# Performance work log

Measured on AMD Instinct MI355X. Metric: run time of the kernel, lower is better.

The kernel has to match this reference:

```python
import jax, jax.numpy as jnp
import numpy as np

N_NODES = 100000
N_EDGES = 1600000
D = 128
N_GRAPHS = 128
N_LAYERS = 3


def setup_inputs() -> dict:
    key = jax.random.key(0)
    ks = jax.random.split(key, 3 + 4 * N_LAYERS)
    x = jax.random.normal(ks[0], (N_NODES, D), dtype=jnp.float32)
    edge_index = jax.random.randint(ks[1], (2, N_EDGES), 0, N_NODES, dtype=jnp.int64)
    batch = jnp.sort(jax.random.randint(ks[2], (N_NODES,), 0, N_GRAPHS, dtype=jnp.int64))
    inp = {"x": x, "edge_index": edge_index, "batch": batch}
    scale = 1.0 / np.sqrt(D)
    for l in range(N_LAYERS):
        inp[f"W1_{l}"] = jax.random.normal(ks[3 + 4 * l], (D, D), dtype=jnp.float32) * scale
        inp[f"b1_{l}"] = jnp.zeros((D,), dtype=jnp.float32)
        inp[f"W2_{l}"] = jax.random.normal(ks[4 + 4 * l], (D, D), dtype=jnp.float32) * scale
        inp[f"b2_{l}"] = jnp.zeros((D,), dtype=jnp.float32)
    return inp


def _gin_conv(x, edge_index, W1, b1, W2, b2):
    # GINConv with eps=0: out = MLP(x + sum_{j in N(i)} x_j)
    msgs = x[edge_index[0]]                                   # [E, D] gather
    agg = jax.ops.segment_sum(msgs, edge_index[1], num_segments=N_NODES)
    h = x + agg
    h = jax.nn.relu(h @ W1 + b1)
    return h @ W2 + b2


def reference(x, edge_index, batch,
              W1_0, b1_0, W2_0, b2_0,
              W1_1, b1_1, W2_1, b2_1,
              W1_2, b1_2, W2_2, b2_2):
    params = [(W1_0, b1_0, W2_0, b2_0), (W1_1, b1_1, W2_1, b2_1), (W1_2, b1_2, W2_2, b2_2)]
    h = x
    for l in range(N_LAYERS - 1):
        h = _gin_conv(h, edge_index, *params[l])
        h = jax.nn.relu(h)  # act; dropout with drop_ratio=0 is identity
    node_emb = _gin_conv(h, edge_index, *params[-1])  # JK='last'
    # global_mean_pool
    sums = jax.ops.segment_sum(node_emb, batch, num_segments=N_GRAPHS)
    counts = jax.ops.segment_sum(jnp.ones((N_NODES, 1), node_emb.dtype), batch, num_segments=N_GRAPHS)
    graph_emb = sums / jnp.maximum(counts, 1.0)
    return graph_emb
```

## Files before the change

### kernel.cpp

```cpp
#include <hip/hip_runtime.h>
#include <hip/hip_bf16.h>

#define N_NODES 100000
#define N_PAD   100032
#define N_EDGES 1600000
#define DIM 128
#define N_GRAPHS 128
#define NBKT 98
#define BSTRIDE 18432
#define TILES (N_PAD / 16)
#define GRID_MLP 1024
#define POOL_BLKS ((N_NODES + 127) / 128)
#define B1_BATCH 4096
#define B1_GRID ((N_EDGES + B1_BATCH - 1) / B1_BATCH)

typedef unsigned short u16;
typedef unsigned int u32;
typedef __attribute__((ext_vector_type(8))) short bf16x8;
typedef __attribute__((ext_vector_type(4))) float f32x4;

#define MFMA(A, B, C) __builtin_amdgcn_mfma_f32_16x16x32_bf16(A, B, C, 0, 0, 0)

__device__ __forceinline__ u16 f2bf(float x) {
    u32 u = __float_as_uint(x);
    u = (u + 0x7FFFu + ((u >> 16) & 1u)) >> 16;
    return (u16)u;
}
__device__ __forceinline__ float bf2f(u16 u) {
    return __uint_as_float(((u32)u) << 16);
}

__global__ __launch_bounds__(256) void bucket1_kernel(const int* __restrict__ src,
                                                      const int* __restrict__ dst,
                                                      u32* __restrict__ cursorB,
                                                      u32* __restrict__ pairs) {
    __shared__ int lh[NBKT];
    __shared__ u32 lbase[NBKT];
    int t = threadIdx.x;
    if (t < NBKT) lh[t] = 0;
    __syncthreads();
    int e0 = blockIdx.x * B1_BATCH;
    int d[16], s[16], rk[16];
#pragma unroll
    for (int k = 0; k < 16; ++k) {
        int e = e0 + t + k * 256;
        if (e < N_EDGES) {
            d[k] = dst[e];
            s[k] = src[e];
            rk[k] = atomicAdd(&lh[d[k] >> 10], 1);
        }
    }
    __syncthreads();
    if (t < NBKT) lbase[t] = atomicAdd(&cursorB[t], (u32)lh[t]) + (u32)(t * BSTRIDE);
    __syncthreads();
#pragma unroll
    for (int k = 0; k < 16; ++k) {
        int e = e0 + t + k * 256;
        if (e < N_EDGES) {
            u32 pos = lbase[d[k] >> 10] + (u32)rk[k];
            pairs[pos] = ((u32)(d[k] & 1023) << 22) | (u32)s[k];
        }
    }
}

__global__ __launch_bounds__(1024) void bucket2_kernel(const u32* __restrict__ cursorB,
                                                       const u32* __restrict__ pairs,
                                                       int* __restrict__ row_ptr,
                                                       int* __restrict__ csr) {
    __shared__ int lh[1024];
    __shared__ int rc[1024];
    __shared__ int bs[128];
    int b = blockIdx.x, t = threadIdx.x;

    if (t < 128) bs[t] = (t < NBKT) ? (int)cursorB[t] : 0;
    __syncthreads();
    for (int off = 1; off < 128; off <<= 1) {
        int v = (t < 128 && t >= off) ? bs[t - off] : 0;
        __syncthreads();
        if (t < 128) bs[t] += v;
        __syncthreads();
    }
    int cnt = (int)cursorB[b];
    int bbase = (b == 0) ? 0 : bs[b - 1];

    lh[t] = 0;
    __syncthreads();
    const u32* pb = pairs + (size_t)b * BSTRIDE;
    for (int i = t; i < cnt; i += 1024) atomicAdd(&lh[__builtin_nontemporal_load(pb + i) >> 22], 1);
    __syncthreads();

    int own = lh[t];
    for (int off = 1; off < 1024; off <<= 1) {
        int v = (t >= off) ? lh[t - off] : 0;
        __syncthreads();
        lh[t] += v;
        __syncthreads();
    }
    int excl = lh[t] - own;
    int node = b * 1024 + t;
    if (node < N_NODES) row_ptr[node] = bbase + excl;
    if (b == 0 && t == 0) row_ptr[N_NODES] = N_EDGES;
    rc[t] = bbase + excl;
    __syncthreads();

    for (int i = t; i < cnt; i += 1024) {
        u32 p = __builtin_nontemporal_load(pb + i);
        int pos = atomicAdd(&rc[p >> 22], 1);
        csr[pos] = (int)(p & 0x3FFFFFu);
    }
}

__global__ __launch_bounds__(256) void xprep_kernel(const float* __restrict__ x,
                                                    u16* __restrict__ hb) {
    int i = blockIdx.x * 256 + threadIdx.x;
    if (i < N_NODES * 32) {
        float4 v = ((const float4*)x)[i];
        ushort4 o;
        o.x = f2bf(v.x); o.y = f2bf(v.y); o.z = f2bf(v.z); o.w = f2bf(v.w);
        ((ushort4*)hb)[i] = o;
    }
}

__global__ __launch_bounds__(256) void agg_kernel(const u16* __restrict__ hb,
                                                  const int* __restrict__ rp,
                                                  const int* __restrict__ csr,
                                                  u16* __restrict__ Ah,
                                                  u16* __restrict__ Al) {
    int node = (blockIdx.x * 256 + threadIdx.x) >> 5;
    int l = threadIdx.x & 31;
    if (node >= N_NODES) return;
    const ushort4* h4 = (const ushort4*)hb;
    ushort4 sv = h4[(size_t)node * 32 + l];
    float a0 = bf2f(sv.x), a1 = bf2f(sv.y), a2 = bf2f(sv.z), a3 = bf2f(sv.w);
    int s = rp[node], e = rp[node + 1];
    int i = s;
    for (; i + 8 <= e; i += 8) {
        ushort4 v0 = h4[(size_t)csr[i + 0] * 32 + l];
        ushort4 v1 = h4[(size_t)csr[i + 1] * 32 + l];
        ushort4 v2 = h4[(size_t)csr[i + 2] * 32 + l];
        ushort4 v3 = h4[(size_t)csr[i + 3] * 32 + l];
        ushort4 v4 = h4[(size_t)csr[i + 4] * 32 + l];
        ushort4 v5 = h4[(size_t)csr[i + 5] * 32 + l];
        ushort4 v6 = h4[(size_t)csr[i + 6] * 32 + l];
        ushort4 v7 = h4[(size_t)csr[i + 7] * 32 + l];
        a0 += ((bf2f(v0.x) + bf2f(v1.x)) + (bf2f(v2.x) + bf2f(v3.x))) +
              ((bf2f(v4.x) + bf2f(v5.x)) + (bf2f(v6.x) + bf2f(v7.x)));
        a1 += ((bf2f(v0.y) + bf2f(v1.y)) + (bf2f(v2.y) + bf2f(v3.y))) +
              ((bf2f(v4.y) + bf2f(v5.y)) + (bf2f(v6.y) + bf2f(v7.y)));
        a2 += ((bf2f(v0.z) + bf2f(v1.z)) + (bf2f(v2.z) + bf2f(v3.z))) +
              ((bf2f(v4.z) + bf2f(v5.z)) + (bf2f(v6.z) + bf2f(v7.z)));
        a3 += ((bf2f(v0.w) + bf2f(v1.w)) + (bf2f(v2.w) + bf2f(v3.w))) +
              ((bf2f(v4.w) + bf2f(v5.w)) + (bf2f(v6.w) + bf2f(v7.w)));
    }
    for (; i < e; ++i) {
        ushort4 v = h4[(size_t)csr[i] * 32 + l];
        a0 += bf2f(v.x); a1 += bf2f(v.y); a2 += bf2f(v.z); a3 += bf2f(v.w);
    }
    ushort4 hv, lv;
    hv.x = f2bf(a0); lv.x = f2bf(a0 - bf2f(hv.x));
    hv.y = f2bf(a1); lv.y = f2bf(a1 - bf2f(hv.y));
    hv.z = f2bf(a2); lv.z = f2bf(a2 - bf2f(hv.z));
    hv.w = f2bf(a3); lv.w = f2bf(a3 - bf2f(hv.w));
    *(ushort4*)(Ah + (size_t)node * 128 + l * 4) = hv;
    *(ushort4*)(Al + (size_t)node * 128 + l * 4) = lv;
}

struct WPrepArgs {
    const float* w[6];
    u16* buf[6];
};
__global__ __launch_bounds__(256) void wprep_kernel(WPrepArgs p) {
    int m = blockIdx.y;
    int idx = blockIdx.x * 256 + threadIdx.x;
    int n = idx >> 7, k = idx & 127;
    float v = p.w[m][k * 128 + n];
    u16 hi = f2bf(v);
    p.buf[m][idx] = hi;
    p.buf[m][idx + 16384] = f2bf(v - bf2f(hi));
}

#define HS 136
__global__ __launch_bounds__(256, 2) void fused_mlp(const u16* __restrict__ Ah,
                                                    const u16* __restrict__ Al,
                                                    const u16* __restrict__ W1,
                                                    const float* __restrict__ b1,
                                                    const u16* __restrict__ W2,
                                                    const float* __restrict__ b2,
                                                    float* __restrict__ Cf,
                                                    u16* __restrict__ Cb, int mode) {
    __shared__ u16 Hh[32 * HS];
    __shared__ u16 Hl[32 * HS];
    int tid = threadIdx.x;
    int lane = tid & 63, wave = tid >> 6;
    int m16 = lane & 15, quad = lane >> 4;
    int colBase = wave * 32;

    bf16x8 W1H[2][4], W1L[2][4], W2H[2][4], W2L[2][4];
#pragma unroll
    for (int nt = 0; nt < 2; ++nt) {
        int n = colBase + nt * 16 + m16;
#pragma unroll
        for (int kb = 0; kb < 4; ++kb) {
            int off = n * 128 + kb * 32 + quad * 8;
            W1H[nt][kb] = *(const bf16x8*)(W1 + off);
            W1L[nt][kb] = *(const bf16x8*)(W1 + off + 16384);
            W2H[nt][kb] = *(const bf16x8*)(W2 + off);
            W2L[nt][kb] = *(const bf16x8*)(W2 + off + 16384);
        }
    }
    float b1v[2][4], b2v[2][4];
#pragma unroll
    for (int nt = 0; nt < 2; ++nt)
#pragma unroll
        for (int rg = 0; rg < 4; ++rg) {
            int col = colBase + nt * 16 + quad * 4 + rg;
            b1v[nt][rg] = b1[col];
            b2v[nt][rg] = b2[col];
        }

    f32x4 z = {0.f, 0.f, 0.f, 0.f};
    bf16x8 aH[2][4], aL[2][4];

    int t0 = blockIdx.x * 2;
    if (t0 < TILES) {
#pragma unroll
        for (int p = 0; p < 2; ++p) {
            const u16* ah = Ah + (size_t)((t0 + p) * 16 + m16) * 128 + quad * 8;
            const u16* al = Al + (size_t)((t0 + p) * 16 + m16) * 128 + quad * 8;
#pragma unroll
            for (int kb = 0; kb < 4; ++kb) {
                aH[p][kb] = *(const bf16x8*)(ah + kb * 32);
                aL[p][kb] = *(const bf16x8*)(al + kb * 32);
            }
        }
    }

    for (; t0 < TILES; t0 += 2 * GRID_MLP) {
        f32x4 acc[2][2];
        acc[0][0] = z; acc[0][1] = z; acc[1][0] = z; acc[1][1] = z;

#pragma unroll
        for (int kb = 0; kb < 4; ++kb) {
#pragma unroll
            for (int p = 0; p < 2; ++p) {
                acc[p][0] = MFMA(W1H[0][kb], aH[p][kb], acc[p][0]);
                acc[p][1] = MFMA(W1H[1][kb], aH[p][kb], acc[p][1]);
                acc[p][0] = MFMA(W1H[0][kb], aL[p][kb], acc[p][0]);
                acc[p][1] = MFMA(W1H[1][kb], aL[p][kb], acc[p][1]);
                acc[p][0] = MFMA(W1L[0][kb], aH[p][kb], acc[p][0]);
                acc[p][1] = MFMA(W1L[1][kb], aH[p][kb], acc[p][1]);
            }
        }

        __syncthreads();

#pragma unroll
        for (int p = 0; p < 2; ++p) {
#pragma unroll
            for (int nt = 0; nt < 2; ++nt) {
                ushort4 hv, lv;
#pragma unroll
                for (int rg = 0; rg < 4; ++rg) {
                    float v = fmaxf(acc[p][nt][rg] + b1v[nt][rg], 0.f);
                    u16 hi = f2bf(v);
                    ((u16*)&hv)[rg] = hi;
                    ((u16*)&lv)[rg] = f2bf(v - bf2f(hi));
                }
                int off = (p * 16 + m16) * HS + colBase + nt * 16 + quad * 4;
                *(ushort4*)&Hh[off] = hv;
                *(ushort4*)&Hl[off] = lv;
            }
        }
        __syncthreads();

        int nt0 = t0 + 2 * GRID_MLP;
        if (nt0 < TILES) {
#pragma unroll
            for (int p = 0; p < 2; ++p) {
                const u16* ah = Ah + (size_t)((nt0 + p) * 16 + m16) * 128 + quad * 8;
                const u16* al = Al + (size_t)((nt0 + p) * 16 + m16) * 128 + quad * 8;
#pragma unroll
                for (int kb = 0; kb < 4; ++kb) {
                    aH[p][kb] = *(const bf16x8*)(ah + kb * 32);
                    aL[p][kb] = *(const bf16x8*)(al + kb * 32);
                }
            }
        }

        f32x4 acc2[2][2];
        acc2[0][0] = z; acc2[0][1] = z; acc2[1][0] = z; acc2[1][1] = z;
#pragma unroll
        for (int kb = 0; kb < 4; ++kb) {
#pragma unroll
            for (int p = 0; p < 2; ++p) {
                int off = (p * 16 + m16) * HS + kb * 32 + quad * 8;
                bf16x8 hH = *(const bf16x8*)(&Hh[off]);
                bf16x8 hL = *(const bf16x8*)(&Hl[off]);
                acc2[p][0] = MFMA(W2H[0][kb], hH, acc2[p][0]);
                acc2[p][1] = MFMA(W2H[1][kb], hH, acc2[p][1]);
                acc2[p][0] = MFMA(W2H[0][kb], hL, acc2[p][0]);
                acc2[p][1] = MFMA(W2H[1][kb], hL, acc2[p][1]);
                acc2[p][0] = MFMA(W2L[0][kb], hH, acc2[p][0]);
                acc2[p][1] = MFMA(W2L[1][kb], hH, acc2[p][1]);
            }
        }

#pragma unroll
        for (int p = 0; p < 2; ++p) {
            size_t row = (size_t)(t0 + p) * 16 + m16;
#pragma unroll
            for (int nt = 0; nt < 2; ++nt) {
                int col = colBase + nt * 16 + quad * 4;
                if (mode) {
                    ushort4 o;
#pragma unroll
                    for (int rg = 0; rg < 4; ++rg)
                        ((u16*)&o)[rg] = f2bf(fmaxf(acc2[p][nt][rg] + b2v[nt][rg], 0.f));
                    *(ushort4*)(Cb + row * 128 + col) = o;
                } else {
                    float4 o;
                    o.x = acc2[p][nt][0] + b2v[nt][0];
                    o.y = acc2[p][nt][1] + b2v[nt][1];
                    o.z = acc2[p][nt][2] + b2v[nt][2];
                    o.w = acc2[p][nt][3] + b2v[nt][3];
                    *(float4*)(Cf + row * 128 + col) = o;
                }
            }
        }
    }
}

__global__ __launch_bounds__(256) void psum_kernel(const float* __restrict__ h,
                                                   const int* __restrict__ batch,
                                                   float* __restrict__ sums) {
    __shared__ int sBatch[128];
    int blk = blockIdx.x, t = threadIdx.x;
    int n0 = blk * 128;
    int nEnd = min(n0 + 128, N_NODES);
    if (t < 128 && n0 + t < N_NODES) sBatch[t] = batch[n0 + t];
    __syncthreads();

    int j = t & 127;
    int half = t >> 7;
    int s = n0 + half * 64;
    int e = min(s + 64, nEnd);

    float acc = 0.f;
    int cur = -1;
    for (int n = s; n < e; ++n) {
        int g = sBatch[n - n0];
        if (g != cur) {
            if (cur >= 0) atomicAdd(&sums[cur * 128 + j], acc);
            cur = g;
            acc = 0.f;
        }
        acc += h[(size_t)n * 128 + j];
    }
    if (cur >= 0) atomicAdd(&sums[cur * 128 + j], acc);
}

__global__ __launch_bounds__(128) void pdiv_kernel(const float* __restrict__ sums,
                                                   const int* __restrict__ batch,
                                                   float* __restrict__ out) {
    __shared__ int sB[2];
    int g = blockIdx.x;
    if (threadIdx.x < 2) {
        int target = g + threadIdx.x;
        int lo = 0, hi = N_NODES;
        while (lo < hi) {
            int m = (lo + hi) >> 1;
            if (batch[m] < target) lo = m + 1; else hi = m;
        }
        sB[threadIdx.x] = lo;
    }
    __syncthreads();
    float cnt = (float)(sB[1] - sB[0]);
    out[g * 128 + threadIdx.x] = sums[g * 128 + threadIdx.x] / fmaxf(cnt, 1.f);
}

extern "C" void kernel_launch(void* const* d_in, const int* in_sizes, int n_in,
                              void* d_out, int out_size, void* d_ws, size_t ws_size,
                              hipStream_t stream) {
    const float* x     = (const float*)d_in[0];
    const int*   ei    = (const int*)d_in[1];
    const int*   batch = (const int*)d_in[2];
    const int*   eSrc  = ei;
    const int*   eDst  = ei + N_EDGES;

    const float* W1[3] = {(const float*)d_in[3], (const float*)d_in[7],  (const float*)d_in[11]};
    const float* b1[3] = {(const float*)d_in[4], (const float*)d_in[8],  (const float*)d_in[12]};
    const float* W2[3] = {(const float*)d_in[5], (const float*)d_in[9],  (const float*)d_in[13]};
    const float* b2[3] = {(const float*)d_in[6], (const float*)d_in[10], (const float*)d_in[14]};

    float* P2 = (float*)d_ws;
    u16*   hb = (u16*)(P2 + (size_t)N_PAD * DIM);
    u16*   Ah = hb + (size_t)N_PAD * DIM;
    u16*   Al = Ah + (size_t)N_PAD * DIM;
    u16*   Wb = Al + (size_t)N_PAD * DIM;
    int*   row_ptr = (int*)(Wb + 6 * 32768);
    u32*   cursorB = (u32*)(row_ptr + N_NODES + 8);
    int*   csr     = (int*)(cursorB + 128);
    float* sums    = (float*)(csr + N_EDGES);
    u32*   pairs   = (u32*)P2;

    hipMemsetAsync(cursorB, 0, 128 * sizeof(u32), stream);
    bucket1_kernel<<<B1_GRID, 256, 0, stream>>>(eSrc, eDst, cursorB, pairs);
    bucket2_kernel<<<NBKT, 1024, 0, stream>>>(cursorB, pairs, row_ptr, csr);

    xprep_kernel<<<(N_NODES * 32 + 255) / 256, 256, 0, stream>>>(x, hb);
    WPrepArgs wp;
    for (int l = 0; l < 3; ++l) {
        wp.w[2 * l]       = W1[l];
        wp.w[2 * l + 1]   = W2[l];
        wp.buf[2 * l]     = Wb + (size_t)(2 * l) * 32768;
        wp.buf[2 * l + 1] = Wb + (size_t)(2 * l + 1) * 32768;
    }
    wprep_kernel<<<dim3(64, 6), 256, 0, stream>>>(wp);
    hipMemsetAsync(sums, 0, N_GRAPHS * DIM * sizeof(float), stream);

    const int aggGrid = (N_NODES * 32 + 255) / 256;

    for (int l = 0; l < 3; ++l) {
        agg_kernel<<<aggGrid, 256, 0, stream>>>(hb, row_ptr, csr, Ah, Al);
        fused_mlp<<<GRID_MLP, 256, 0, stream>>>(Ah, Al,
                                                Wb + (size_t)(2 * l) * 32768, b1[l],
                                                Wb + (size_t)(2 * l + 1) * 32768, b2[l],
                                                P2, hb, (l < 2) ? 1 : 0);
    }
    psum_kernel<<<POOL_BLKS, 256, 0, stream>>>(P2, batch, sums);
    pdiv_kernel<<<N_GRAPHS, 128, 0, stream>>>(sums, batch, (float*)d_out);
}
```

Measured before the change: 532.1 us.

## Drop low-half bf16 split of aggregated activations and process four tiles per block

The aggregation kernel now writes only the bf16 high part of the summed features, so the separate low-residual buffer and its stores and loads are removed. The first MLP GEMM goes from three MFMA passes to two (W-hi×A and W-lo×A). The fused MLP block also handles four 16-row tiles per iteration instead of two, with larger shared buffers. This cuts memory traffic and MFMA work, but at the cost of precision in the first layer's input, and raises register and LDS use, which may lower occupancy.

```diff
diff --git a/kernel.cpp b/kernel.cpp
--- a/kernel.cpp
+++ b/kernel.cpp
@@ -124,8 +124,7 @@
 __global__ __launch_bounds__(256) void agg_kernel(const u16* __restrict__ hb,
                                                   const int* __restrict__ rp,
                                                   const int* __restrict__ csr,
-                                                  u16* __restrict__ Ah,
-                                                  u16* __restrict__ Al) {
+                                                  u16* __restrict__ Ah) {
     int node = (blockIdx.x * 256 + threadIdx.x) >> 5;
     int l = threadIdx.x & 31;
     if (node >= N_NODES) return;
@@ -156,13 +155,9 @@
         ushort4 v = h4[(size_t)csr[i] * 32 + l];
         a0 += bf2f(v.x); a1 += bf2f(v.y); a2 += bf2f(v.z); a3 += bf2f(v.w);
     }
-    ushort4 hv, lv;
-    hv.x = f2bf(a0); lv.x = f2bf(a0 - bf2f(hv.x));
-    hv.y = f2bf(a1); lv.y = f2bf(a1 - bf2f(hv.y));
-    hv.z = f2bf(a2); lv.z = f2bf(a2 - bf2f(hv.z));
-    hv.w = f2bf(a3); lv.w = f2bf(a3 - bf2f(hv.w));
+    ushort4 hv;
+    hv.x = f2bf(a0); hv.y = f2bf(a1); hv.z = f2bf(a2); hv.w = f2bf(a3);
     *(ushort4*)(Ah + (size_t)node * 128 + l * 4) = hv;
-    *(ushort4*)(Al + (size_t)node * 128 + l * 4) = lv;
 }
 
 struct WPrepArgs {
@@ -181,15 +176,14 @@
 
 #define HS 136
 __global__ __launch_bounds__(256, 2) void fused_mlp(const u16* __restrict__ Ah,
-                                                    const u16* __restrict__ Al,
                                                     const u16* __restrict__ W1,
                                                     const float* __restrict__ b1,
                                                     const u16* __restrict__ W2,
                                                     const float* __restrict__ b2,
                                                     float* __restrict__ Cf,
                                                     u16* __restrict__ Cb, int mode) {
-    __shared__ u16 Hh[32 * HS];
-    __shared__ u16 Hl[32 * HS];
+    __shared__ u16 Hh[64 * HS];
+    __shared__ u16 Hl[64 * HS];
     int tid = threadIdx.x;
     int lane = tid & 63, wave = tid >> 6;
     int m16 = lane & 15, quad = lane >> 4;
@@ -219,34 +213,30 @@
         }
 
     f32x4 z = {0.f, 0.f, 0.f, 0.f};
-    bf16x8 aH[2][4], aL[2][4];
-
-    int t0 = blockIdx.x * 2;
+    bf16x8 aH[4][4];
+
+    int t0 = blockIdx.x * 4;
     if (t0 < TILES) {
 #pragma unroll
-        for (int p = 0; p < 2; ++p) {
+        for (int p = 0; p < 4; ++p) {
             const u16* ah = Ah + (size_t)((t0 + p) * 16 + m16) * 128 + quad * 8;
-            const u16* al = Al + (size_t)((t0 + p) * 16 + m16) * 128 + quad * 8;
-#pragma unroll
-            for (int kb = 0; kb < 4; ++kb) {
+#pragma unroll
+            for (int kb = 0; kb < 4; ++kb)
                 aH[p][kb] = *(const bf16x8*)(ah + kb * 32);
-                aL[p][kb] = *(const bf16x8*)(al + kb * 32);
-            }
-        }
-    }
-
-    for (; t0 < TILES; t0 += 2 * GRID_MLP) {
-        f32x4 acc[2][2];
-        acc[0][0] = z; acc[0][1] = z; acc[1][0] = z; acc[1][1] = z;
+        }
+    }
+
+    for (; t0 < TILES; t0 += 4 * GRID_MLP) {
+        f32x4 acc[4][2];
+#pragma unroll
+        for (int p = 0; p < 4; ++p) { acc[p][0] = z; acc[p][1] = z; }
 
 #pragma unroll
         for (int kb = 0; kb < 4; ++kb) {
 #pragma unroll
-            for (int p = 0; p < 2; ++p) {
+            for (int p = 0; p < 4; ++p) {
                 acc[p][0] = MFMA(W1H[0][kb], aH[p][kb], acc[p][0]);
                 acc[p][1] = MFMA(W1H[1][kb], aH[p][kb], acc[p][1]);
-                acc[p][0] = MFMA(W1H[0][kb], aL[p][kb], acc[p][0]);
-                acc[p][1] = MFMA(W1H[1][kb], aL[p][kb], acc[p][1]);
                 acc[p][0] = MFMA(W1L[0][kb], aH[p][kb], acc[p][0]);
                 acc[p][1] = MFMA(W1L[1][kb], aH[p][kb], acc[p][1]);
             }
@@ -255,7 +245,7 @@
         __syncthreads();
 
 #pragma unroll
-        for (int p = 0; p < 2; ++p) {
+        for (int p = 0; p < 4; ++p) {
 #pragma unroll
             for (int nt = 0; nt < 2; ++nt) {
                 ushort4 hv, lv;
@@ -273,26 +263,24 @@
         }
         __syncthreads();
 
-        int nt0 = t0 + 2 * GRID_MLP;
+        int nt0 = t0 + 4 * GRID_MLP;
         if (nt0 < TILES) {
 #pragma unroll
-            for (int p = 0; p < 2; ++p) {
+            for (int p = 0; p < 4; ++p) {
                 const u16* ah = Ah + (size_t)((nt0 + p) * 16 + m16) * 128 + quad * 8;
-                const u16* al = Al + (size_t)((nt0 + p) * 16 + m16) * 128 + quad * 8;
-#pragma unroll
-                for (int kb = 0; kb < 4; ++kb) {
+#pragma unroll
+                for (int kb = 0; kb < 4; ++kb)
                     aH[p][kb] = *(const bf16x8*)(ah + kb * 32);
-                    aL[p][kb] = *(const bf16x8*)(al + kb * 32);
-                }
             }
         }
 
-        f32x4 acc2[2][2];
-        acc2[0][0] = z; acc2[0][1] = z; acc2[1][0] = z; acc2[1][1] = z;
+        f32x4 acc2[4][2];
+#pragma unroll
+        for (int p = 0; p < 4; ++p) { acc2[p][0] = z; acc2[p][1] = z; }
 #pragma unroll
         for (int kb = 0; kb < 4; ++kb) {
 #pragma unroll
-            for (int p = 0; p < 2; ++p) {
+            for (int p = 0; p < 4; ++p) {
                 int off = (p * 16 + m16) * HS + kb * 32 + quad * 8;
                 bf16x8 hH = *(const bf16x8*)(&Hh[off]);
                 bf16x8 hL = *(const bf16x8*)(&Hl[off]);
@@ -306,7 +294,7 @@
         }
 
 #pragma unroll
-        for (int p = 0; p < 2; ++p) {
+        for (int p = 0; p < 4; ++p) {
             size_t row = (size_t)(t0 + p) * 16 + m16;
 #pragma unroll
             for (int nt = 0; nt < 2; ++nt) {
@@ -395,8 +383,7 @@
     float* P2 = (float*)d_ws;
     u16*   hb = (u16*)(P2 + (size_t)N_PAD * DIM);
     u16*   Ah = hb + (size_t)N_PAD * DIM;
-    u16*   Al = Ah + (size_t)N_PAD * DIM;
-    u16*   Wb = Al + (size_t)N_PAD * DIM;
+    u16*   Wb = Ah + (size_t)N_PAD * DIM;
     int*   row_ptr = (int*)(Wb + 6 * 32768);
     u32*   cursorB = (u32*)(row_ptr + N_NODES + 8);
     int*   csr     = (int*)(cursorB + 128);
@@ -421,8 +408,8 @@
     const int aggGrid = (N_NODES * 32 + 255) / 256;
 
     for (int l = 0; l < 3; ++l) {
-        agg_kernel<<<aggGrid, 256, 0, stream>>>(hb, row_ptr, csr, Ah, Al);
-        fused_mlp<<<GRID_MLP, 256, 0, stream>>>(Ah, Al,
+        agg_kernel<<<aggGrid, 256, 0, stream>>>(hb, row_ptr, csr, Ah);
+        fused_mlp<<<GRID_MLP, 256, 0, stream>>>(Ah,
                                                 Wb + (size_t)(2 * l) * 32768, b1[l],
                                                 Wb + (size_t)(2 * l + 1) * 32768, b2[l],
                                                 P2, hb, (l < 2) ? 1 : 0);
```

After: 514.9 us. 1.03x faster.
